# Optimization experiments

Hardware: AMD Instinct MI355X
Metric: run time of the kernel (lower is better)

The kernel has to match this reference:

```python
import jax, jax.numpy as jnp
import numpy as np

B, T, D, H = 1024, 200, 64, 64


def setup_inputs() -> dict:
    key = jax.random.key(0)
    ks = jax.random.split(key, 24)
    s = 0.05
    inp = {
        'dense_inputs': jax.random.normal(ks[0], (B, 4), jnp.float32),
        'sparse_inputs': jax.random.randint(ks[1], (B, 2), 0, 1000),
        'seq_inputs': jax.random.randint(ks[2], (B, T, 1), 0, 1000000),
        'item_inputs': jax.random.randint(ks[3], (B, 1), 0, 1000000),
        'hist_len': jax.random.randint(ks[4], (B,), 1, T + 1),
        'item_table': jax.random.normal(ks[5], (1000000, D), jnp.float32) * s,
        'other_tables': jax.random.normal(ks[6], (2, 1000, 16), jnp.float32) * s,
        'gru_W': jax.random.normal(ks[7], (D, 3 * H), jnp.float32) * s,
        'gru_U': jax.random.normal(ks[8], (H, 3 * H), jnp.float32) * s,
        'gru_b': jnp.zeros((3 * H,), jnp.float32),
        'aug_W': jax.random.normal(ks[9], (H, 3 * H), jnp.float32) * s,
        'aug_U': jax.random.normal(ks[10], (H, 3 * H), jnp.float32) * s,
        'aug_b': jnp.zeros((3 * H,), jnp.float32),
        'att_W1': jax.random.normal(ks[11], (4 * D, 64), jnp.float32) * s,
        'att_b1': jnp.zeros((64,), jnp.float32),
        'att_W2': jax.random.normal(ks[12], (64, 16), jnp.float32) * s,
        'att_b2': jnp.zeros((16,), jnp.float32),
        'att_W3': jax.random.normal(ks[13], (16, 1), jnp.float32) * s,
        'att_b3': jnp.zeros((1,), jnp.float32),
        'ffn_W1': jax.random.normal(ks[14], (164, 256), jnp.float32) * s,
        'ffn_b1': jnp.zeros((256,), jnp.float32),
        'ffn_W2': jax.random.normal(ks[15], (256, 128), jnp.float32) * s,
        'ffn_b2': jnp.zeros((128,), jnp.float32),
        'ffn_W3': jax.random.normal(ks[16], (128, 64), jnp.float32) * s,
        'ffn_b3': jnp.zeros((64,), jnp.float32),
        'out_W': jax.random.normal(ks[17], (64, 1), jnp.float32) * s,
        'out_b': jnp.zeros((1,), jnp.float32),
    }
    return inp


def _gru_scan(x_tbd, valid_tb, W, U, b, att_tb=None):
    """Masked (AU)GRU scan. x_tbd: [T,B,D]; valid_tb: [T,B] bool; att_tb: [T,B] or None.
    Returns (final_state [B,H], seq_states [T,B,H])."""
    h0 = jnp.zeros((x_tbd.shape[1], H), x_tbd.dtype)

    def step(h, inp):
        x, valid, a = inp
        xw = x @ W + b            # [B,3H]
        hu = h @ U                # [B,3H]
        z = jax.nn.sigmoid(xw[:, :H] + hu[:, :H])
        r = jax.nn.sigmoid(xw[:, H:2 * H] + hu[:, H:2 * H])
        hh = jnp.tanh(xw[:, 2 * H:] + r * hu[:, 2 * H:])
        if a is not None:
            z = a[:, None] * z    # AUGRU: attention-scaled update gate
        h_new = (1.0 - z) * h + z * hh
        h = jnp.where(valid[:, None], h_new, h)
        return h, h

    xs = (x_tbd, valid_tb, att_tb)
    if att_tb is None:
        def step2(h, inp):
            return step(h, (inp[0], inp[1], None))
        return jax.lax.scan(step2, h0, (x_tbd, valid_tb))
    return jax.lax.scan(step, h0, xs)


def _dice(x):
    # Dice activation at alpha=0: p=sigmoid(batch-standardized x); out = p*x
    m = jnp.mean(x, axis=0, keepdims=True)
    v = jnp.var(x, axis=0, keepdims=True)
    p = jax.nn.sigmoid((x - m) * jax.lax.rsqrt(v + 1e-9))
    return p * x


def reference(dense_inputs, sparse_inputs, seq_inputs, item_inputs, hist_len,
              item_table, other_tables, gru_W, gru_U, gru_b, aug_W, aug_U, aug_b,
              att_W1, att_b1, att_W2, att_b2, att_W3, att_b3,
              ffn_W1, ffn_b1, ffn_W2, ffn_b2, ffn_W3, ffn_b3, out_W, out_b):
    # Embedding lookups
    seq_embed = item_table[seq_inputs[:, :, 0]]          # [B,T,D]
    target_embed = item_table[item_inputs[:, 0]]         # [B,D]
    other = jnp.concatenate([other_tables[i][sparse_inputs[:, i]] for i in range(2)], axis=-1)  # [B,32]
    other_info = jnp.concatenate([dense_inputs, other], axis=-1)  # [B,36]

    valid_tb = jnp.arange(T)[:, None] < hist_len[None, :]  # [T,B]

    # Interest extraction: plain GRU over behavior sequence
    _, seq_h_tbh = _gru_scan(jnp.transpose(seq_embed, (1, 0, 2)), valid_tb, gru_W, gru_U, gru_b)
    seq_h = jnp.transpose(seq_h_tbh, (1, 0, 2))           # [B,T,H]

    # DIN-style target attention: MLP over [q, k, q-k, q*k]
    qt = jnp.broadcast_to(target_embed[:, None, :], seq_h.shape)
    feats = jnp.concatenate([qt, seq_h, qt - seq_h, qt * seq_h], axis=-1)  # [B,T,4D]
    prelu = lambda x: jnp.where(x > 0, x, 0.25 * x)
    a = prelu(feats @ att_W1 + att_b1)
    a = prelu(a @ att_W2 + att_b2)
    logits = (a @ att_W3 + att_b3)[..., 0]                # [B,T]
    logits = jnp.where(valid_tb.T, logits, -1e9)
    scores = jax.nn.softmax(logits, axis=-1)              # [B,T]

    # Interest evolution: AUGRU gated by attention scores
    final_state, _ = _gru_scan(seq_h_tbh, valid_tb, aug_W, aug_U, aug_b, att_tb=scores.T)

    out = jnp.concatenate([final_state, target_embed, other_info], axis=-1)  # [B,164]
    out = _dice(out @ ffn_W1 + ffn_b1)
    out = _dice(out @ ffn_W2 + ffn_b2)
    out = _dice(out @ ffn_W3 + ffn_b3)
    out = jax.nn.sigmoid(out @ out_W + out_b)             # [B,1]
    return out
```

## Files before the change

### kernel.cpp

```cpp
#include <hip/hip_runtime.h>

#define BB 1024
#define TT 200

typedef __attribute__((ext_vector_type(8))) short short8;
typedef __attribute__((ext_vector_type(2))) short short2v;
typedef __attribute__((ext_vector_type(4))) float f32x4;

__device__ __forceinline__ float sigmoidf_(float x) { return __fdividef(1.0f, 1.0f + __expf(-x)); }
__device__ __forceinline__ float tanh_fast(float x) {
    x = fminf(15.f, fmaxf(-15.f, x));
    float e = __expf(-2.f * x);
    return __fdividef(1.f - e, 1.f + e);
}
__device__ __forceinline__ float dicef_(float x, float m, float v) {
    return x * sigmoidf_((x - m) * rsqrtf(v + 1e-9f));
}
__device__ __forceinline__ unsigned short f2bf(float f) {
    unsigned u = __float_as_uint(f);
    unsigned r = u + 0x7fffu + ((u >> 16) & 1u);
    return (unsigned short)(r >> 16);
}
__device__ __forceinline__ float bf2f(unsigned short h) {
    return __uint_as_float(((unsigned)h) << 16);
}
__device__ __forceinline__ unsigned cvt_pk_bf16(float lo, float hi) {
    unsigned r;
    asm("v_cvt_pk_bf16_f32 %0, %1, %2" : "=v"(r) : "v"(lo), "v"(hi));
    return r;
}
union U8 { short8 s8; unsigned u[4]; };

#if __has_builtin(__builtin_amdgcn_fdot2_f32_bf16)
__device__ __forceinline__ float dot2bf(unsigned h2, unsigned u2, float c) {
    union { unsigned u; short2v s; } A, B;
    A.u = h2; B.u = u2;
    return __builtin_amdgcn_fdot2_f32_bf16(A.s, B.s, c, false);
}
#else
__device__ __forceinline__ float dot2bf(unsigned h2, unsigned u2, float c) {
    float h0 = __uint_as_float(h2 << 16), h1 = __uint_as_float(h2 & 0xffff0000u);
    float u0 = __uint_as_float(u2 << 16), u1 = __uint_as_float(u2 & 0xffff0000u);
    return fmaf(h1, u1, fmaf(h0, u0, c));
}
#endif

__global__ void k_prep(const float* __restrict__ dense, const int* __restrict__ sparse,
                       const int* __restrict__ item_idx, const float* __restrict__ table,
                       const float* __restrict__ other_tables,
                       float* __restrict__ target, float* __restrict__ other) {
    int b = blockIdx.x, l = threadIdx.x;
    target[b * 64 + l] = table[(size_t)item_idx[b] * 64 + l];
    if (l < 4) other[b * 36 + l] = dense[b * 4 + l];
    else if (l < 20) other[b * 36 + l] = other_tables[(size_t)sparse[b * 2 + 0] * 16 + (l - 4)];
    else if (l < 36) other[b * 36 + l] = other_tables[1000 * 16 + (size_t)sparse[b * 2 + 1] * 16 + (l - 20)];
}

template <int GATHER>
__global__ __launch_bounds__(256, 1) void k_xw(
    const int* __restrict__ idx, const float* __restrict__ tablef,
    const unsigned short* __restrict__ Abf,
    const float* __restrict__ W, const float* __restrict__ bias,
    const int* __restrict__ hist_len,
    unsigned short* __restrict__ out, int Mtiles, int tilestride)
{
    const int l = threadIdx.x & 63;
    const int wv = threadIdx.x >> 6;
    const int lg = l >> 4;
    const int li = l & 15;

    short8 bfr[12][2];
    float bn[12];
#pragma unroll
    for (int nt = 0; nt < 12; ++nt) {
        bn[nt] = bias[nt * 16 + li];
#pragma unroll
        for (int c = 0; c < 2; ++c) {
#pragma unroll
            for (int j = 0; j < 8; ++j) {
                int k = c * 32 + lg * 8 + j;
                bfr[nt][c][j] = (short)f2bf(W[k * 192 + nt * 16 + li]);
            }
        }
    }

    for (int tile = blockIdx.x * 4 + wv; tile < Mtiles; tile += tilestride) {
        long row = (long)tile * 16 + li;
        {
            int bb = (int)(row / TT);
            int tt = (int)(row - (long)bb * TT);
            int vld = (tt < hist_len[bb]) ? 1 : 0;
            if (__ballot(vld) == 0ull) continue;
        }

        short8 a[2];
        if (GATHER) {
            long id = idx[row];
            const float* tp = tablef + id * 64 + lg * 8;
#pragma unroll
            for (int c = 0; c < 2; ++c) {
                f32x4 v0 = *(const f32x4*)(tp + c * 32);
                f32x4 v1 = *(const f32x4*)(tp + c * 32 + 4);
#pragma unroll
                for (int j = 0; j < 4; ++j) {
                    a[c][j] = (short)f2bf(v0[j]);
                    a[c][4 + j] = (short)f2bf(v1[j]);
                }
            }
        } else {
#pragma unroll
            for (int c = 0; c < 2; ++c)
                a[c] = *(const short8*)(Abf + row * 64 + c * 32 + lg * 8);
        }

        f32x4 acc[12];
#pragma unroll
        for (int nt = 0; nt < 12; ++nt) acc[nt] = (f32x4){0.f, 0.f, 0.f, 0.f};
#pragma unroll
        for (int c = 0; c < 2; ++c)
#pragma unroll
            for (int nt = 0; nt < 12; ++nt)
                acc[nt] = __builtin_amdgcn_mfma_f32_16x16x32_bf16(a[c], bfr[nt][c], acc[nt], 0, 0, 0);

#pragma unroll
        for (int nt = 0; nt < 12; ++nt)
#pragma unroll
            for (int j = 0; j < 4; ++j) {
                long orow = (long)tile * 16 + lg * 4 + j;
                out[orow * 192 + nt * 16 + li] = f2bf(acc[nt][j] + bn[nt]);
            }
    }
}

template <int AUG>
__global__ __launch_bounds__(64, 1) void k_scan10(
    const unsigned short* __restrict__ xw,
    const float* __restrict__ U,
    const int* __restrict__ hist_len,
    const float* __restrict__ scores,
    unsigned short* __restrict__ hout,
    float* __restrict__ hfinal)
{
    __shared__ unsigned Ul[64 * 96];
    __shared__ unsigned hb[32];
    const int l = threadIdx.x;
    const int b = blockIdx.x;
    const int len = hist_len[b];
    const unsigned sw = ((unsigned)l & 7u) << 2;

    unsigned* rowp = Ul + l * 96;
    for (int kk = 0; kk < 32; ++kk) {
        unsigned pz = cvt_pk_bf16(U[(2 * kk) * 192 + l],       U[(2 * kk + 1) * 192 + l]);
        unsigned pr = cvt_pk_bf16(U[(2 * kk) * 192 + 64 + l],  U[(2 * kk + 1) * 192 + 64 + l]);
        unsigned ph = cvt_pk_bf16(U[(2 * kk) * 192 + 128 + l], U[(2 * kk + 1) * 192 + 128 + l]);
        rowp[(kk ^ sw)]      = pz;
        rowp[32 + (kk ^ sw)] = pr;
        rowp[64 + (kk ^ sw)] = ph;
    }

    const unsigned short* xwr = xw + (size_t)b * TT * 192;
    const float* scr = scores + (size_t)b * TT;
    unsigned short* hor = hout + (size_t)b * TT * 64;

    unsigned short* hbs = (unsigned short*)hb;
    float h = 0.f;
    hbs[l] = 0;

    unsigned short nz = xwr[l], nr = xwr[64 + l], nh = xwr[128 + l];
    float ns = AUG ? scr[0] : 0.f;

    const uint4* H4 = (const uint4*)hb;

    for (int t = 0; t < len; ++t) {
        const unsigned short cz = nz, cr = nr, ch = nh;
        const float cs = ns;
        if (t + 1 < len) {
            const unsigned short* p = xwr + (size_t)(t + 1) * 192;
            nz = p[l]; nr = p[64 + l]; nh = p[128 + l];
            if (AUG) ns = scr[t + 1];
        }

        float az0 = 0.f, az1 = 0.f, ar0 = 0.f, ar1 = 0.f, ah0 = 0.f, ah1 = 0.f;
#pragma unroll
        for (int q = 0; q < 8; ++q) {
            uint4 hq = H4[q];
            uint4 uz = *(const uint4*)(rowp + ((4 * q) ^ sw));
            uint4 ur = *(const uint4*)(rowp + 32 + ((4 * q) ^ sw));
            uint4 uh = *(const uint4*)(rowp + 64 + ((4 * q) ^ sw));
            az0 = dot2bf(hq.x, uz.x, az0);
            ar0 = dot2bf(hq.x, ur.x, ar0);
            ah0 = dot2bf(hq.x, uh.x, ah0);
            az1 = dot2bf(hq.y, uz.y, az1);
            ar1 = dot2bf(hq.y, ur.y, ar1);
            ah1 = dot2bf(hq.y, uh.y, ah1);
            az0 = dot2bf(hq.z, uz.z, az0);
            ar0 = dot2bf(hq.z, ur.z, ar0);
            ah0 = dot2bf(hq.z, uh.z, ah0);
            az1 = dot2bf(hq.w, uz.w, az1);
            ar1 = dot2bf(hq.w, ur.w, ar1);
            ah1 = dot2bf(hq.w, uh.w, ah1);
        }
        float azf = az0 + az1, arf = ar0 + ar1, ahf = ah0 + ah1;

        float zg = sigmoidf_(bf2f(cz) + azf);
        if (AUG) zg *= cs;
        float rg = sigmoidf_(bf2f(cr) + arf);
        float hv = tanh_fast(bf2f(ch) + rg * ahf);
        h = (1.f - zg) * h + zg * hv;

        const unsigned short hbf = f2bf(h);
        hbs[l] = hbf;
        if (!AUG) hor[(size_t)t * 64 + l] = hbf;
    }

    if (AUG) {
        hfinal[(size_t)b * 64 + l] = h;
    } else {
        const unsigned short fro = f2bf(h);
        for (int t = len; t < TT; ++t) hor[(size_t)t * 64 + l] = fro;
    }
}

__global__ __launch_bounds__(256, 2) void k_att(
    const float* __restrict__ target, const unsigned short* __restrict__ seq_hb,
    const float* __restrict__ W1, const float* __restrict__ b1,
    const float* __restrict__ W2, const float* __restrict__ b2,
    const float* __restrict__ W3, const float* __restrict__ b3,
    const int* __restrict__ hist_len, float* __restrict__ scores)
{
    __shared__ unsigned short W1f[8 * 4 * 64 * 8];
    __shared__ float a1s[4][16][68];
    __shared__ float logit_lds[208];
    __shared__ float red[8];

    const int tid = threadIdx.x;
    const int wv = tid >> 6, l = tid & 63;
    const int lg = l >> 4, li = l & 15;
    const int b = blockIdx.x;
    const int len = hist_len[b];

    if (tid < 208) logit_lds[tid] = -1e9f;
    for (int i = tid; i < 8 * 4 * 64 * 8; i += 256) {
        int j = i & 7, ll = (i >> 3) & 63, nt = (i >> 9) & 3, c = i >> 11;
        int k = c * 32 + (ll >> 4) * 8 + j;
        int col = nt * 16 + (ll & 15);
        W1f[i] = f2bf(W1[k * 64 + col]);
    }
    __syncthreads();

    short8 w1r[8][4];
    const short8* wf = (const short8*)W1f;
#pragma unroll
    for (int c = 0; c < 8; ++c)
#pragma unroll
        for (int nt = 0; nt < 4; ++nt)
            w1r[c][nt] = wf[(c * 4 + nt) * 64 + l];

    short8 w2r[2];
#pragma unroll
    for (int c = 0; c < 2; ++c) {
        U8 t8;
#pragma unroll
        for (int m = 0; m < 4; ++m) {
            int k0 = c * 32 + lg * 8 + 2 * m;
            t8.u[m] = cvt_pk_bf16(W2[k0 * 16 + li], W2[(k0 + 1) * 16 + li]);
        }
        w2r[c] = t8.s8;
    }

    float b1v[4];
#pragma unroll
    for (int nt = 0; nt < 4; ++nt) b1v[nt] = b1[nt * 16 + li];
    const float b2v = b2[li];
    const float w3v = W3[li];
    const float b3r = b3[0];

    const float* qp = target + (size_t)b * 64;
    float qf_lo[8], qf_hi[8];
#pragma unroll
    for (int j = 0; j < 8; ++j) { qf_lo[j] = qp[lg * 8 + j]; qf_hi[j] = qp[32 + lg * 8 + j]; }
    U8 q8l, q8h;
#pragma unroll
    for (int m = 0; m < 4; ++m) {
        q8l.u[m] = cvt_pk_bf16(qf_lo[2 * m], qf_lo[2 * m + 1]);
        q8h.u[m] = cvt_pk_bf16(qf_hi[2 * m], qf_hi[2 * m + 1]);
    }

    for (int mt = wv; mt * 16 < len; mt += 4) {
        const int t = mt * 16 + li;
        const int tld = (t < TT) ? t : TT - 1;
        const unsigned short* hp = seq_hb + ((size_t)b * TT + tld) * 64 + lg * 8;
        short8 h8l = *(const short8*)hp;
        short8 h8h = *(const short8*)(hp + 32);

        U8 d8l, d8h, m8l, m8h;
#pragma unroll
        for (int m = 0; m < 4; ++m) {
            float h0, h1, d0, d1, p0, p1;
            h0 = bf2f((unsigned short)h8l[2 * m]); h1 = bf2f((unsigned short)h8l[2 * m + 1]);
            d0 = qf_lo[2 * m] - h0; d1 = qf_lo[2 * m + 1] - h1;
            p0 = qf_lo[2 * m] * h0; p1 = qf_lo[2 * m + 1] * h1;
            d8l.u[m] = cvt_pk_bf16(d0, d1);
            m8l.u[m] = cvt_pk_bf16(p0, p1);
            h0 = bf2f((unsigned short)h8h[2 * m]); h1 = bf2f((unsigned short)h8h[2 * m + 1]);
            d0 = qf_hi[2 * m] - h0; d1 = qf_hi[2 * m + 1] - h1;
            p0 = qf_hi[2 * m] * h0; p1 = qf_hi[2 * m + 1] * h1;
            d8h.u[m] = cvt_pk_bf16(d0, d1);
            m8h.u[m] = cvt_pk_bf16(p0, p1);
        }

        f32x4 acc[4];
#pragma unroll
        for (int nt = 0; nt < 4; ++nt) acc[nt] = (f32x4){0.f, 0.f, 0.f, 0.f};
#pragma unroll
        for (int nt = 0; nt < 4; ++nt) {
            acc[nt] = __builtin_amdgcn_mfma_f32_16x16x32_bf16(q8l.s8, w1r[0][nt], acc[nt], 0, 0, 0);
            acc[nt] = __builtin_amdgcn_mfma_f32_16x16x32_bf16(q8h.s8, w1r[1][nt], acc[nt], 0, 0, 0);
            acc[nt] = __builtin_amdgcn_mfma_f32_16x16x32_bf16(h8l,    w1r[2][nt], acc[nt], 0, 0, 0);
            acc[nt] = __builtin_amdgcn_mfma_f32_16x16x32_bf16(h8h,    w1r[3][nt], acc[nt], 0, 0, 0);
            acc[nt] = __builtin_amdgcn_mfma_f32_16x16x32_bf16(d8l.s8, w1r[4][nt], acc[nt], 0, 0, 0);
            acc[nt] = __builtin_amdgcn_mfma_f32_16x16x32_bf16(d8h.s8, w1r[5][nt], acc[nt], 0, 0, 0);
            acc[nt] = __builtin_amdgcn_mfma_f32_16x16x32_bf16(m8l.s8, w1r[6][nt], acc[nt], 0, 0, 0);
            acc[nt] = __builtin_amdgcn_mfma_f32_16x16x32_bf16(m8h.s8, w1r[7][nt], acc[nt], 0, 0, 0);
        }

#pragma unroll
        for (int nt = 0; nt < 4; ++nt)
#pragma unroll
            for (int jj = 0; jj < 4; ++jj) {
                float v = acc[nt][jj] + b1v[nt];
                a1s[wv][lg * 4 + jj][nt * 16 + li] = (v > 0.f) ? v : 0.25f * v;
            }

        const float* arow = &a1s[wv][li][0];
        f32x4 acc2 = (f32x4){0.f, 0.f, 0.f, 0.f};
#pragma unroll
        for (int c2 = 0; c2 < 2; ++c2) {
            f32x4 v0 = *(const f32x4*)(arow + c2 * 32 + lg * 8);
            f32x4 v1 = *(const f32x4*)(arow + c2 * 32 + lg * 8 + 4);
            U8 a2f;
            a2f.u[0] = cvt_pk_bf16(v0[0], v0[1]);
            a2f.u[1] = cvt_pk_bf16(v0[2], v0[3]);
            a2f.u[2] = cvt_pk_bf16(v1[0], v1[1]);
            a2f.u[3] = cvt_pk_bf16(v1[2], v1[3]);
            acc2 = __builtin_amdgcn_mfma_f32_16x16x32_bf16(a2f.s8, w2r[c2], acc2, 0, 0, 0);
        }

#pragma unroll
        for (int jj = 0; jj < 4; ++jj) {
            float a2 = acc2[jj] + b2v;
            a2 = (a2 > 0.f) ? a2 : 0.25f * a2;
            float part = a2 * w3v;
            part += __shfl_xor(part, 1);
            part += __shfl_xor(part, 2);
            part += __shfl_xor(part, 4);
            part += __shfl_xor(part, 8);
            int tt = mt * 16 + lg * 4 + jj;
            if (li == 0 && tt < TT)
                logit_lds[tt] = (tt < len) ? (part + b3r) : -1e9f;
        }
    }
    __syncthreads();

    float v = (tid < TT) ? logit_lds[tid] : -1e30f;
    float m = v;
#pragma unroll
    for (int s = 1; s < 64; s <<= 1) m = fmaxf(m, __shfl_xor(m, s));
    if (l == 0) red[wv] = m;
    __syncthreads();
    m = fmaxf(fmaxf(red[0], red[1]), fmaxf(red[2], red[3]));
    float e = (tid < TT) ? __expf(v - m) : 0.f;
    float sum = e;
#pragma unroll
    for (int s = 1; s < 64; s <<= 1) sum += __shfl_xor(sum, s);
    if (l == 0) red[4 + wv] = sum;
    __syncthreads();
    float inv = __fdividef(1.f, red[4] + red[5] + red[6] + red[7]);
    if (tid < TT) scores[(size_t)b * TT + tid] = e * inv;
}

__global__ __launch_bounds__(256) void k_fc1(const float* __restrict__ fin,
                                             const float* __restrict__ tgt,
                                             const float* __restrict__ oth,
                                             const float* __restrict__ Wt,
                                             const float* __restrict__ bvec,
                                             float* __restrict__ fout) {
    __shared__ float z0[164];
    int b = blockIdx.x, tid = threadIdx.x;
    if (tid < 64) z0[tid] = fin[b * 64 + tid];
    else if (tid < 128) z0[tid] = tgt[b * 64 + tid - 64];
    else if (tid < 164) z0[tid] = oth[b * 36 + tid - 128];
    __syncthreads();
    float acc = bvec[tid];
#pragma unroll 4
    for (int k = 0; k < 164; ++k) acc += z0[k] * Wt[k * 256 + tid];
    fout[(size_t)b * 256 + tid] = acc;
}

template <int F>
__global__ __launch_bounds__(256) void k_stats(const float* __restrict__ x, float* __restrict__ stat) {
    int c = blockIdx.x, tid = threadIdx.x;
    float s = 0.f, sq = 0.f;
    for (int i = tid; i < BB; i += 256) {
        float v = x[(size_t)i * F + c];
        s += v; sq += v * v;
    }
#pragma unroll
    for (int m = 1; m < 64; m <<= 1) { s += __shfl_xor(s, m); sq += __shfl_xor(sq, m); }
    __shared__ float rs[4], rq[4];
    if ((tid & 63) == 0) { rs[tid >> 6] = s; rq[tid >> 6] = sq; }
    __syncthreads();
    if (tid == 0) {
        float S = rs[0] + rs[1] + rs[2] + rs[3];
        float Q = rq[0] + rq[1] + rq[2] + rq[3];
        float mean = S * (1.f / BB);
        float var = Q * (1.f / BB) - mean * mean;
        stat[c] = mean;
        stat[F + c] = var;
    }
}

__global__ __launch_bounds__(256) void k_fc2(const float* __restrict__ f1,
                                             const float* __restrict__ st1,
                                             const float* __restrict__ Wt,
                                             const float* __restrict__ bvec,
                                             float* __restrict__ f2) {
    __shared__ float z[256];
    int b = blockIdx.x, tid = threadIdx.x;
    float x = f1[(size_t)b * 256 + tid];
    z[tid] = dicef_(x, st1[tid], st1[256 + tid]);
    __syncthreads();
    if (tid < 128) {
        float acc = bvec[tid];
#pragma unroll 4
        for (int k = 0; k < 256; ++k) acc += z[k] * Wt[k * 128 + tid];
        f2[(size_t)b * 128 + tid] = acc;
    }
}

__global__ __launch_bounds__(128) void k_fc3(const float* __restrict__ f2,
                                             const float* __restrict__ st2,
                                             const float* __restrict__ Wt,
                                             const float* __restrict__ bvec,
                                             float* __restrict__ f3) {
    __shared__ float z[128];
    int b = blockIdx.x, tid = threadIdx.x;
    float x = f2[(size_t)b * 128 + tid];
    z[tid] = dicef_(x, st2[tid], st2[128 + tid]);
    __syncthreads();
    if (tid < 64) {
        float acc = bvec[tid];
#pragma unroll 4
        for (int k = 0; k < 128; ++k) acc += z[k] * Wt[k * 64 + tid];
        f3[(size_t)b * 64 + tid] = acc;
    }
}

__global__ void k_out(const float* __restrict__ f3, const float* __restrict__ st3,
                      const float* __restrict__ outW, const float* __restrict__ outb,
                      float* __restrict__ out) {
    int b = blockIdx.x, l = threadIdx.x;
    float x = f3[(size_t)b * 64 + l];
    float z = dicef_(x, st3[l], st3[64 + l]);
    float p = z * outW[l];
#pragma unroll
    for (int m = 1; m < 64; m <<= 1) p += __shfl_xor(p, m);
    if (l == 0) out[b] = sigmoidf_(p + outb[0]);
}

extern "C" void kernel_launch(void* const* d_in, const int* in_sizes, int n_in,
                              void* d_out, int out_size, void* d_ws, size_t ws_size,
                              hipStream_t stream) {
    const float* dense      = (const float*)d_in[0];
    const int*   sparse     = (const int*)d_in[1];
    const int*   seq_idx    = (const int*)d_in[2];
    const int*   item_idx   = (const int*)d_in[3];
    const int*   hist_len   = (const int*)d_in[4];
    const float* item_table = (const float*)d_in[5];
    const float* other_tab  = (const float*)d_in[6];
    const float* gru_W = (const float*)d_in[7];
    const float* gru_U = (const float*)d_in[8];
    const float* gru_b = (const float*)d_in[9];
    const float* aug_W = (const float*)d_in[10];
    const float* aug_U = (const float*)d_in[11];
    const float* aug_b = (const float*)d_in[12];
    const float* att_W1 = (const float*)d_in[13];
    const float* att_b1 = (const float*)d_in[14];
    const float* att_W2 = (const float*)d_in[15];
    const float* att_b2 = (const float*)d_in[16];
    const float* att_W3 = (const float*)d_in[17];
    const float* att_b3 = (const float*)d_in[18];
    const float* ffn_W1 = (const float*)d_in[19];
    const float* ffn_b1 = (const float*)d_in[20];
    const float* ffn_W2 = (const float*)d_in[21];
    const float* ffn_b2 = (const float*)d_in[22];
    const float* ffn_W3 = (const float*)d_in[23];
    const float* ffn_b3 = (const float*)d_in[24];
    const float* out_W  = (const float*)d_in[25];
    const float* out_b  = (const float*)d_in[26];

    float* wsf = (float*)d_ws;
    unsigned short* xwb   = (unsigned short*)(wsf);
    unsigned short* seqhb = (unsigned short*)(wsf + 19660800);
    float* scores = wsf + 26214400;
    float* target = wsf + 26419200;
    float* other  = wsf + 26484736;
    float* finals = wsf + 26521600;
    float* f1     = wsf + 26587136;
    float* f2     = wsf + 26849280;
    float* f3     = wsf + 26980352;
    float* st1    = wsf + 27045888;
    float* st2    = wsf + 27046400;
    float* st3    = wsf + 27046656;

    float* dout = (float*)d_out;
    const int Mtiles = (BB * TT) / 16;

    k_prep<<<BB, 64, 0, stream>>>(dense, sparse, item_idx, item_table, other_tab, target, other);

    k_xw<1><<<800, 256, 0, stream>>>(seq_idx, item_table, nullptr, gru_W, gru_b, hist_len, xwb, Mtiles, 3200);

    k_scan10<0><<<BB, 64, 0, stream>>>(xwb, gru_U, hist_len, scores, seqhb, finals);

    k_att<<<BB, 256, 0, stream>>>(target, seqhb, att_W1, att_b1, att_W2, att_b2,
                                  att_W3, att_b3, hist_len, scores);

    k_xw<0><<<800, 256, 0, stream>>>(nullptr, nullptr, seqhb, aug_W, aug_b, hist_len, xwb, Mtiles, 3200);

    k_scan10<1><<<BB, 64, 0, stream>>>(xwb, aug_U, hist_len, scores, seqhb, finals);

    k_fc1<<<BB, 256, 0, stream>>>(finals, target, other, ffn_W1, ffn_b1, f1);
    k_stats<256><<<256, 256, 0, stream>>>(f1, st1);
    k_fc2<<<BB, 256, 0, stream>>>(f1, st1, ffn_W2, ffn_b2, f2);
    k_stats<128><<<128, 256, 0, stream>>>(f2, st2);
    k_fc3<<<BB, 128, 0, stream>>>(f2, st2, ffn_W3, ffn_b3, f3);
    k_stats<64><<<64, 256, 0, stream>>>(f3, st3);
    k_out<<<BB, 64, 0, stream>>>(f3, st3, out_W, out_b, dout);
}
```

Baseline: 406.7 us.

## Store xw time-major per gate-lane and chunk-prefetch 8 steps in GRU scans

```diff
diff --git a/kernel.cpp b/kernel.cpp
--- a/kernel.cpp
+++ b/kernel.cpp
@@ -122,18 +122,25 @@
             for (int nt = 0; nt < 12; ++nt)
                 acc[nt] = __builtin_amdgcn_mfma_f32_16x16x32_bf16(a[c], bfr[nt][c], acc[nt], 0, 0, 0);
 
-#pragma unroll
-        for (int nt = 0; nt < 12; ++nt)
-#pragma unroll
-            for (int j = 0; j < 4; ++j) {
-                long orow = (long)tile * 16 + lg * 4 + j;
-                out[orow * 192 + nt * 16 + li] = f2bf(acc[nt][j] + bn[nt]);
+        {
+            long r0 = (long)tile * 16 + lg * 4;
+            int bb = (int)(r0 / TT);
+            int tt = (int)(r0 - (long)bb * TT);
+#pragma unroll
+            for (int nt = 0; nt < 12; ++nt) {
+                int g = nt >> 2;
+                int cc = (nt & 3) * 16 + li;
+                uint2 pk;
+                pk.x = cvt_pk_bf16(acc[nt][0] + bn[nt], acc[nt][1] + bn[nt]);
+                pk.y = cvt_pk_bf16(acc[nt][2] + bn[nt], acc[nt][3] + bn[nt]);
+                *(uint2*)(out + ((size_t)(bb * 3 + g) * 64 + cc) * TT + tt) = pk;
             }
+        }
     }
 }
 
 template <int AUG>
-__global__ __launch_bounds__(64, 1) void k_scan10(
+__global__ __launch_bounds__(64, 1) void k_scan13(
     const unsigned short* __restrict__ xw,
     const float* __restrict__ U,
     const int* __restrict__ hist_len,
@@ -158,28 +165,19 @@
         rowp[64 + (kk ^ sw)] = ph;
     }
 
-    const unsigned short* xwr = xw + (size_t)b * TT * 192;
+    const unsigned short* zp = xw + ((size_t)(b * 3 + 0) * 64 + l) * TT;
+    const unsigned short* rp = xw + ((size_t)(b * 3 + 1) * 64 + l) * TT;
+    const unsigned short* hp = xw + ((size_t)(b * 3 + 2) * 64 + l) * TT;
     const float* scr = scores + (size_t)b * TT;
     unsigned short* hor = hout + (size_t)b * TT * 64;
 
     unsigned short* hbs = (unsigned short*)hb;
     float h = 0.f;
     hbs[l] = 0;
-
-    unsigned short nz = xwr[l], nr = xwr[64 + l], nh = xwr[128 + l];
-    float ns = AUG ? scr[0] : 0.f;
-
     const uint4* H4 = (const uint4*)hb;
 
-    for (int t = 0; t < len; ++t) {
-        const unsigned short cz = nz, cr = nr, ch = nh;
-        const float cs = ns;
-        if (t + 1 < len) {
-            const unsigned short* p = xwr + (size_t)(t + 1) * 192;
-            nz = p[l]; nr = p[64 + l]; nh = p[128 + l];
-            if (AUG) ns = scr[t + 1];
-        }
-
+    auto stepf = [&](unsigned short cz, unsigned short cr, unsigned short ch,
+                     float cs, int t) {
         float az0 = 0.f, az1 = 0.f, ar0 = 0.f, ar1 = 0.f, ah0 = 0.f, ah1 = 0.f;
 #pragma unroll
         for (int q = 0; q < 8; ++q) {
@@ -206,18 +204,53 @@
         if (AUG) zg *= cs;
         float rg = sigmoidf_(bf2f(cr) + arf);
         float hv = tanh_fast(bf2f(ch) + rg * ahf);
-        h = (1.f - zg) * h + zg * hv;
+        float hn = (1.f - zg) * h + zg * hv;
+        h = (t < len) ? hn : h;
 
         const unsigned short hbf = f2bf(h);
         hbs[l] = hbf;
-        if (!AUG) hor[(size_t)t * 64 + l] = hbf;
-    }
+        if (!AUG && t < len) hor[(size_t)t * 64 + l] = hbf;
+    };
+
+    const int nch = (len + 7) >> 3;
+    short8 zA = {}, rA = {}, hA = {}, zB = {}, rB = {}, hB = {};
+    f32x4 sA0 = (f32x4){0.f, 0.f, 0.f, 0.f}, sA1 = sA0, sB0 = sA0, sB1 = sA0;
+
+#define LOADC(sfx, c) { \
+        z##sfx = *(const short8*)(zp + (size_t)(c) * 8); \
+        r##sfx = *(const short8*)(rp + (size_t)(c) * 8); \
+        h##sfx = *(const short8*)(hp + (size_t)(c) * 8); \
+        if (AUG) { s##sfx##0 = *(const f32x4*)(scr + (c) * 8); \
+                   s##sfx##1 = *(const f32x4*)(scr + (c) * 8 + 4); } }
+
+#define PROC(sfx, c) { const int t0_ = (c) * 8; \
+        stepf((unsigned short)z##sfx[0], (unsigned short)r##sfx[0], (unsigned short)h##sfx[0], s##sfx##0[0], t0_ + 0); \
+        stepf((unsigned short)z##sfx[1], (unsigned short)r##sfx[1], (unsigned short)h##sfx[1], s##sfx##0[1], t0_ + 1); \
+        stepf((unsigned short)z##sfx[2], (unsigned short)r##sfx[2], (unsigned short)h##sfx[2], s##sfx##0[2], t0_ + 2); \
+        stepf((unsigned short)z##sfx[3], (unsigned short)r##sfx[3], (unsigned short)h##sfx[3], s##sfx##0[3], t0_ + 3); \
+        stepf((unsigned short)z##sfx[4], (unsigned short)r##sfx[4], (unsigned short)h##sfx[4], s##sfx##1[0], t0_ + 4); \
+        stepf((unsigned short)z##sfx[5], (unsigned short)r##sfx[5], (unsigned short)h##sfx[5], s##sfx##1[1], t0_ + 5); \
+        stepf((unsigned short)z##sfx[6], (unsigned short)r##sfx[6], (unsigned short)h##sfx[6], s##sfx##1[2], t0_ + 6); \
+        stepf((unsigned short)z##sfx[7], (unsigned short)r##sfx[7], (unsigned short)h##sfx[7], s##sfx##1[3], t0_ + 7); }
+
+    LOADC(A, 0)
+    for (int c = 0; c < nch; c += 2) {
+        if (c + 1 < nch) LOADC(B, c + 1)
+        PROC(A, c)
+        if (c + 1 < nch) {
+            if (c + 2 < nch) LOADC(A, c + 2)
+            PROC(B, c + 1)
+        }
+    }
+
+#undef LOADC
+#undef PROC
 
     if (AUG) {
         hfinal[(size_t)b * 64 + l] = h;
     } else {
         const unsigned short fro = f2bf(h);
-        for (int t = len; t < TT; ++t) hor[(size_t)t * 64 + l] = fro;
+        for (int tt = len; tt < TT; ++tt) hor[(size_t)tt * 64 + l] = fro;
     }
 }
 
@@ -520,14 +553,14 @@
 
     k_xw<1><<<800, 256, 0, stream>>>(seq_idx, item_table, nullptr, gru_W, gru_b, hist_len, xwb, Mtiles, 3200);
 
-    k_scan10<0><<<BB, 64, 0, stream>>>(xwb, gru_U, hist_len, scores, seqhb, finals);
+    k_scan13<0><<<BB, 64, 0, stream>>>(xwb, gru_U, hist_len, scores, seqhb, finals);
 
     k_att<<<BB, 256, 0, stream>>>(target, seqhb, att_W1, att_b1, att_W2, att_b2,
                                   att_W3, att_b3, hist_len, scores);
 
     k_xw<0><<<800, 256, 0, stream>>>(nullptr, nullptr, seqhb, aug_W, aug_b, hist_len, xwb, Mtiles, 3200);
 
-    k_scan10<1><<<BB, 64, 0, stream>>>(xwb, aug_U, hist_len, scores, seqhb, finals);
+    k_scan13<1><<<BB, 64, 0, stream>>>(xwb, aug_U, hist_len, scores, seqhb, finals);
 
     k_fc1<<<BB, 256, 0, stream>>>(finals, target, other, ffn_W1, ffn_b1, f1);
     k_stats<256><<<256, 256, 0, stream>>>(f1, st1);
```

Measured after the change: 582.4 us. 43.2% more time.
